# Kernel optimization log

Measured on AMD Instinct MI355X. Metric: run time of the kernel, lower is better.

## Reference

```python
import jax, jax.numpy as jnp
import numpy as np

B, L, H = 2, 2048, 1024
N_HEADS = 16
HEAD = H // N_HEADS
LN_EPS = 1e-12


def setup_inputs() -> dict:
    key = jax.random.key(0)
    ks = jax.random.split(key, 8)
    s = 1.0 / np.sqrt(H)
    return {
        "embeddings": jax.random.normal(ks[0], (B, L, H), dtype=jnp.float32),
        "mask": jnp.zeros((B, 1, 1, L), dtype=jnp.float32),
        "Wq": jax.random.normal(ks[1], (H, H), dtype=jnp.float32) * s,
        "bq": jnp.zeros((H,), dtype=jnp.float32),
        "Wk": jax.random.normal(ks[2], (H, H), dtype=jnp.float32) * s,
        "bk": jnp.zeros((H,), dtype=jnp.float32),
        "Wv": jax.random.normal(ks[3], (H, H), dtype=jnp.float32) * s,
        "bv": jnp.zeros((H,), dtype=jnp.float32),
        "Wo": jax.random.normal(ks[4], (H, H), dtype=jnp.float32) * s,
        "bo": jnp.zeros((H,), dtype=jnp.float32),
        "ln_gamma": jnp.ones((H,), dtype=jnp.float32),
        "ln_beta": jnp.zeros((H,), dtype=jnp.float32),
    }


def _layer_norm(x, gamma, beta):
    mu = jnp.mean(x, axis=-1, keepdims=True)
    var = jnp.mean(jnp.square(x - mu), axis=-1, keepdims=True)
    return (x - mu) * jax.lax.rsqrt(var + LN_EPS) * gamma + beta


def reference(embeddings, mask, Wq, bq, Wk, bk, Wv, bv, Wo, bo, ln_gamma, ln_beta):
    b, l, h = embeddings.shape
    # QKV projections, split heads -> [b, n_heads, l, head]
    def split_heads(x):
        return x.reshape(b, l, N_HEADS, HEAD).transpose(0, 2, 1, 3)
    q = split_heads(embeddings @ Wq + bq)
    k = split_heads(embeddings @ Wk + bk)
    v = split_heads(embeddings @ Wv + bv)
    # Faithful to source: energies use Q @ V^T, scaled by sqrt(n_heads)
    energies = jnp.einsum("bhqd,bhkd->bhqk", q, v) / np.sqrt(N_HEADS) + mask
    weights = jax.nn.softmax(energies, axis=3)
    # Faithful to source: attended = weights @ K
    attended = jnp.einsum("bhqk,bhkd->bhqd", weights, k)
    attended = attended.transpose(0, 2, 1, 3).reshape(b, l, h)
    # Residual feed-forward (BertSelfOutput style): dense + residual + LN
    out = attended @ Wo + bo
    return _layer_norm(out + embeddings, ln_gamma, ln_beta)
```

## Files before the change

### kernel.cpp

```cpp
#include <hip/hip_runtime.h>

#define LOG2E 1.44269504f
#define C_QSCALE 0.360673760f
#define C_SHIFT  34.6246810f
typedef unsigned short u16;
typedef short bf16x8 __attribute__((ext_vector_type(8)));
typedef float f32x4 __attribute__((ext_vector_type(4)));
typedef unsigned short u16x4 __attribute__((ext_vector_type(4)));

#define BB 2
#define LL 2048
#define HH 1024
#define NH 16
#define HD 64
#define ML (BB*LL)

__device__ __forceinline__ u16 f2bf(float f) {
  union { float f; unsigned u; } v; v.f = f;
  unsigned r = v.u + 0x7FFFu + ((v.u >> 16) & 1u);
  return (u16)(r >> 16);
}
__device__ __forceinline__ u16 f2bf_trunc(float f) {
  union { float f; unsigned u; } v; v.f = f;
  return (u16)(v.u >> 16);
}
__device__ __forceinline__ float bf2f(u16 u) {
  union { unsigned u; float f; } v; v.u = ((unsigned)u) << 16;
  return v.f;
}
__device__ __forceinline__ void gload_lds16(const u16* g, u16* l) {
  __builtin_amdgcn_global_load_lds((const __attribute__((address_space(1))) void*)g,
                                   (__attribute__((address_space(3))) void*)l, 16, 0, 0);
}

__global__ __launch_bounds__(256) void k_prep(const float* __restrict__ E, u16* __restrict__ X,
                                              const float* W0, const float* W1,
                                              const float* W2, const float* W3,
                                              u16* __restrict__ WT) {
  __shared__ __align__(16) u16 T[64*72];
  if (blockIdx.x < 2048) {
    int idx = (blockIdx.x * 256 + threadIdx.x) * 8;
    float4 a = *(const float4*)(E + idx);
    float4 b = *(const float4*)(E + idx + 4);
    bf16x8 o;
    o[0]=f2bf(a.x); o[1]=f2bf(a.y); o[2]=f2bf(a.z); o[3]=f2bf(a.w);
    o[4]=f2bf(b.x); o[5]=f2bf(b.y); o[6]=f2bf(b.z); o[7]=f2bf(b.w);
    *(bf16x8*)(X + idx) = o;
    return;
  }
  int bz = blockIdx.x - 2048;
  int z = bz >> 8, rem = bz & 255, bx = rem & 15, by = rem >> 4;
  const float* W = (z==0)?W0:(z==1)?W1:(z==2)?W2:W3;
  u16* dst = WT + (size_t)z * HH * HH;
  int t = threadIdx.x;
  int n0 = bx * 64, k0 = by * 64;
  int kl = t >> 2, nc = t & 3;
  #pragma unroll
  for (int u = 0; u < 4; ++u) {
    float4 v = *(const float4*)(W + (size_t)(k0 + kl) * HH + n0 + nc*16 + u*4);
    int nb = nc*16 + u*4;
    T[(nb+0)*72 + kl] = f2bf(v.x);
    T[(nb+1)*72 + kl] = f2bf(v.y);
    T[(nb+2)*72 + kl] = f2bf(v.z);
    T[(nb+3)*72 + kl] = f2bf(v.w);
  }
  __syncthreads();
  int nl = t >> 2, kc = (t & 3) * 16;
  #pragma unroll
  for (int e = 0; e < 2; ++e) {
    bf16x8 v = *(const bf16x8*)(T + nl*72 + kc + e*8);
    *(bf16x8*)(dst + (size_t)(n0+nl)*HH + k0 + kc + e*8) = v;
  }
}

__global__ __launch_bounds__(256) void k_gemm(const u16* __restrict__ A, const u16* __restrict__ Bt,
                                              const float* __restrict__ b0, const float* __restrict__ b1,
                                              const float* __restrict__ b2,
                                              u16* __restrict__ QH, u16* __restrict__ KV,
                                              float* __restrict__ outf, int mode) {
  __shared__ __align__(16) u16 As[2][128*32];
  __shared__ __align__(16) u16 Bs[2][128*32];
  int tid = threadIdx.x;
  int lane = tid & 63, w = tid >> 6;
  int c = lane & 15, g = lane >> 4;
  int bn0 = blockIdx.x * 128, bm0 = blockIdx.y * 128;
  int wm0 = (w >> 1) * 64, wn0 = (w & 1) * 64;
  int z = bn0 >> 10;
  bool swapd = (mode == 1) || (z != 1);
  const u16* srcA = swapd ? Bt : A;
  const u16* srcB = swapd ? A : Bt;
  int baseA = swapd ? bn0 : bm0;
  int baseB = swapd ? bm0 : bn0;

  f32x4 acc[4][4];
  #pragma unroll
  for (int mt = 0; mt < 4; ++mt)
    #pragma unroll
    for (int nt = 0; nt < 4; ++nt)
      acc[mt][nt] = (f32x4){0.f,0.f,0.f,0.f};

  #pragma unroll
  for (int it = 0; it < 2; ++it) {
    int ch = tid + it*256, row = ch >> 2, col = (ch & 3) * 8;
    gload_lds16(srcA + (size_t)(baseA + row) * HH + col, &As[0][ch*8]);
    gload_lds16(srcB + (size_t)(baseB + row) * HH + col, &Bs[0][ch*8]);
  }
  for (int kt = 0; kt < 32; ++kt) {
    __syncthreads();
    int cb = kt & 1;
    if (kt < 31) {
      int k0 = (kt + 1) * 32, nb = (kt + 1) & 1;
      #pragma unroll
      for (int it = 0; it < 2; ++it) {
        int ch = tid + it*256, row = ch >> 2, col = (ch & 3) * 8;
        gload_lds16(srcA + (size_t)(baseA + row) * HH + k0 + col, &As[nb][ch*8]);
        gload_lds16(srcB + (size_t)(baseB + row) * HH + k0 + col, &Bs[nb][ch*8]);
      }
    }
    bf16x8 af[4], bfr[4];
    #pragma unroll
    for (int i = 0; i < 4; ++i) {
      af[i]  = *(const bf16x8*)(&As[cb][0] + (wm0 + i*16 + c)*32 + g*8);
      bfr[i] = *(const bf16x8*)(&Bs[cb][0] + (wn0 + i*16 + c)*32 + g*8);
    }
    #pragma unroll
    for (int mt = 0; mt < 4; ++mt)
      #pragma unroll
      for (int nt = 0; nt < 4; ++nt)
        acc[mt][nt] = __builtin_amdgcn_mfma_f32_16x16x32_bf16(af[mt], bfr[nt], acc[mt][nt], 0, 0, 0);
  }

  if (mode == 1) {
    #pragma unroll
    for (int mt = 0; mt < 4; ++mt) {
      int n0 = bn0 + wm0 + mt*16 + 4*g;
      float4 bv = *(const float4*)(b0 + n0);
      #pragma unroll
      for (int nt = 0; nt < 4; ++nt) {
        int tok = bm0 + wn0 + nt*16 + c;
        float4 o;
        o.x = acc[mt][nt][0] + bv.x;
        o.y = acc[mt][nt][1] + bv.y;
        o.z = acc[mt][nt][2] + bv.z;
        o.w = acc[mt][nt][3] + bv.w;
        *(float4*)(outf + (size_t)tok * HH + n0) = o;
      }
    }
  } else if (z == 1) {
    #pragma unroll
    for (int nt = 0; nt < 4; ++nt) {
      int n = bn0 + wn0 + nt*16 + c;
      int nn = n & 1023, h = nn >> 6, d = nn & 63;
      float bv = b1[nn];
      #pragma unroll
      for (int mt = 0; mt < 4; ++mt) {
        int m0 = bm0 + wm0 + mt*16 + 4*g;
        int b = m0 >> 11, keyl = m0 & 2047;
        int tt = keyl >> 6, chunk = (keyl >> 3) & 7, s = keyl & 7;
        u16x4 pk;
        #pragma unroll
        for (int r = 0; r < 4; ++r) pk[r] = f2bf(acc[mt][nt][r] + bv);
        *(u16x4*)(KV + ((size_t)((b*NH + h)*32 + tt))*8192 + d*64 + ((chunk ^ (d & 7))*8) + s) = pk;
      }
    }
  } else {
    #pragma unroll
    for (int mt = 0; mt < 4; ++mt) {
      int nidx0 = bn0 + wm0 + mt*16 + 4*g;
      int nn0 = nidx0 & 1023, h = nn0 >> 6, d0 = nn0 & 63;
      const float* bp = (z == 0) ? b0 : b2;
      float4 bv = *(const float4*)(bp + nn0);
      #pragma unroll
      for (int nt = 0; nt < 4; ++nt) {
        int tok = bm0 + wn0 + nt*16 + c;
        int b = tok >> 11, l = tok & 2047;
        u16x4 o;
        o[0] = f2bf(acc[mt][nt][0] + bv.x);
        o[1] = f2bf(acc[mt][nt][1] + bv.y);
        o[2] = f2bf(acc[mt][nt][2] + bv.z);
        o[3] = f2bf(acc[mt][nt][3] + bv.w);
        if (z == 0) {
          *(u16x4*)(QH + (((size_t)(b*NH + h)) * LL + l) * HD + d0) = o;
        } else {
          int tt = l >> 6;
          *(u16x4*)(KV + ((size_t)((b*NH + h)*32 + tt))*8192 + 4096
                    + (l & 63)*64 + (((d0 >> 3) ^ (l & 7))*8) + (d0 & 7)) = o;
        }
      }
    }
  }
}

__global__ __launch_bounds__(256) void k_attn(const u16* __restrict__ QH, const u16* __restrict__ KV,
                                              const float* __restrict__ mask,
                                              u16* __restrict__ PO, float* __restrict__ PL) {
  __shared__ __align__(16) u16 sKV[8192];
  __shared__ __align__(16) u16 sP[4][32*72];
  int tid = threadIdx.x;
  int lane = tid & 63, w = tid >> 6;
  int c = lane & 15, g = lane >> 4;
  int z = blockIdx.y;
  int bh = blockIdx.z, b = bh >> 4;
  int q0 = blockIdx.x * 128 + w * 32;
  size_t qbase = (size_t)bh * LL * HD;
  const u16* kvg = KV + (size_t)bh * 32 * 8192 + (size_t)z * 16 * 8192;
  const float* mptr = mask + b * LL + z * 1024;
  u16* pw = &sP[w][0];

  bf16x8 aq[2][2];
  #pragma unroll
  for (int qi = 0; qi < 2; ++qi)
    #pragma unroll
    for (int ks = 0; ks < 2; ++ks)
      aq[qi][ks] = *(const bf16x8*)(QH + qbase + (size_t)(q0 + qi*16 + c) * HD + ks*32 + g*8);

  bf16x8 ones;
  #pragma unroll
  for (int i = 0; i < 8; ++i) ones[i] = (short)0x3F80;

  f32x4 O[2][4], lac[2];
  #pragma unroll
  for (int qi = 0; qi < 2; ++qi) {
    lac[qi] = (f32x4){0.f,0.f,0.f,0.f};
    #pragma unroll
    for (int dt = 0; dt < 4; ++dt) O[qi][dt] = (f32x4){0.f,0.f,0.f,0.f};
  }

  for (int tt = 0; tt < 16; ++tt) {
    __syncthreads();
    #pragma unroll
    for (int it = 0; it < 4; ++it) {
      int i = (tid + it*256) * 8;
      gload_lds16(kvg + (size_t)tt*8192 + i, sKV + i);
    }
    __syncthreads();

    int kv0 = tt * 64;
    #pragma unroll
    for (int nt = 0; nt < 4; ++nt) {
      int vrow = nt*16 + c;
      bf16x8 vb0 = *(const bf16x8*)(sKV + 4096 + vrow*64 + ((g ^ (c & 7))*8));
      bf16x8 vb1 = *(const bf16x8*)(sKV + 4096 + vrow*64 + (((4 + g) ^ (c & 7))*8));
      float mterm = fmaf(mptr[kv0 + vrow], LOG2E, -C_SHIFT);
      #pragma unroll
      for (int qi = 0; qi < 2; ++qi) {
        f32x4 sa = (f32x4){0.f,0.f,0.f,0.f};
        sa = __builtin_amdgcn_mfma_f32_16x16x32_bf16(aq[qi][0], vb0, sa, 0,0,0);
        sa = __builtin_amdgcn_mfma_f32_16x16x32_bf16(aq[qi][1], vb1, sa, 0,0,0);
        #pragma unroll
        for (int r = 0; r < 4; ++r)
          pw[(qi*16 + 4*g + r)*72 + nt*16 + c] = f2bf_trunc(exp2f(fmaf(sa[r], C_QSCALE, mterm)));
      }
    }
    bf16x8 ap[2][2];
    #pragma unroll
    for (int qi = 0; qi < 2; ++qi) {
      ap[qi][0] = *(const bf16x8*)(pw + (qi*16 + c)*72 + g*8);
      ap[qi][1] = *(const bf16x8*)(pw + (qi*16 + c)*72 + 32 + g*8);
      lac[qi] = __builtin_amdgcn_mfma_f32_16x16x32_bf16(ones, ap[qi][0], lac[qi], 0,0,0);
      lac[qi] = __builtin_amdgcn_mfma_f32_16x16x32_bf16(ones, ap[qi][1], lac[qi], 0,0,0);
    }
    #pragma unroll
    for (int dt = 0; dt < 4; ++dt) {
      int d = dt*16 + c;
      bf16x8 bk0 = *(const bf16x8*)(sKV + d*64 + ((g ^ (c & 7))*8));
      bf16x8 bk1 = *(const bf16x8*)(sKV + d*64 + (((4 + g) ^ (c & 7))*8));
      #pragma unroll
      for (int qi = 0; qi < 2; ++qi) {
        O[qi][dt] = __builtin_amdgcn_mfma_f32_16x16x32_bf16(bk0, ap[qi][0], O[qi][dt], 0,0,0);
        O[qi][dt] = __builtin_amdgcn_mfma_f32_16x16x32_bf16(bk1, ap[qi][1], O[qi][dt], 0,0,0);
      }
    }
  }
  #pragma unroll
  for (int qi = 0; qi < 2; ++qi) {
    size_t qrow = (size_t)(z*32 + bh) * LL + q0 + qi*16 + c;
    if (g == 0) PL[qrow] = lac[qi][0];
    #pragma unroll
    for (int dt = 0; dt < 4; ++dt) {
      u16x4 o;
      #pragma unroll
      for (int r = 0; r < 4; ++r) o[r] = f2bf(O[qi][dt][r]);
      *(u16x4*)(PO + qrow*HD + dt*16 + 4*g) = o;
    }
  }
}

__global__ __launch_bounds__(256) void k_combine(const u16* __restrict__ PO,
                                                 const float* __restrict__ PL,
                                                 u16* __restrict__ ATT) {
  int bh = blockIdx.y, b = bh >> 4, h = bh & 15;
  int q = blockIdx.x * 128 + (threadIdx.x >> 1);
  int dh = (threadIdx.x & 1) * 32;
  size_t r0 = ((size_t)bh * LL + q) * HD + dh;
  size_t r1 = ((size_t)(32 + bh) * LL + q) * HD + dh;
  float inv = 1.0f / (PL[(size_t)bh * LL + q] + PL[(size_t)(32 + bh) * LL + q]);
  u16* dst = ATT + ((size_t)(b*LL + q)) * HH + h*HD + dh;
  #pragma unroll
  for (int e = 0; e < 4; ++e) {
    bf16x8 a = *(const bf16x8*)(PO + r0 + e*8);
    bf16x8 bb = *(const bf16x8*)(PO + r1 + e*8);
    bf16x8 o;
    #pragma unroll
    for (int i = 0; i < 8; ++i)
      o[i] = (short)f2bf((bf2f((u16)a[i]) + bf2f((u16)bb[i])) * inv);
    *(bf16x8*)(dst + e*8) = o;
  }
}

__global__ __launch_bounds__(256) void k_ln(const float* __restrict__ OF, const float* __restrict__ E,
                                            const float* __restrict__ gamma, const float* __restrict__ beta,
                                            float* __restrict__ out) {
  int row = blockIdx.x;
  int tid = threadIdx.x, lane = tid & 63, w = tid >> 6;
  size_t basei = (size_t)row * HH + tid*4;
  float4 a = *(const float4*)(OF + basei);
  float4 e = *(const float4*)(E + basei);
  float x0 = a.x + e.x, x1 = a.y + e.y, x2 = a.z + e.z, x3 = a.w + e.w;
  float s1 = x0+x1+x2+x3;
  float s2 = x0*x0+x1*x1+x2*x2+x3*x3;
  #pragma unroll
  for (int off = 32; off; off >>= 1) { s1 += __shfl_xor(s1, off); s2 += __shfl_xor(s2, off); }
  __shared__ float r1[4], r2[4];
  if (lane == 0) { r1[w] = s1; r2[w] = s2; }
  __syncthreads();
  s1 = r1[0]+r1[1]+r1[2]+r1[3];
  s2 = r2[0]+r2[1]+r2[2]+r2[3];
  float mu = s1 * (1.0f/HH);
  float var = s2 * (1.0f/HH) - mu*mu;
  float rs = rsqrtf(fmaxf(var, 0.f) + 1e-12f);
  int colb = tid*4;
  float4 gm = *(const float4*)(gamma + colb);
  float4 bt = *(const float4*)(beta + colb);
  float4 o;
  o.x = (x0-mu)*rs*gm.x + bt.x;
  o.y = (x1-mu)*rs*gm.y + bt.y;
  o.z = (x2-mu)*rs*gm.z + bt.z;
  o.w = (x3-mu)*rs*gm.w + bt.w;
  *(float4*)(out + basei) = o;
}

extern "C" void kernel_launch(void* const* d_in, const int* in_sizes, int n_in,
                              void* d_out, int out_size, void* d_ws, size_t ws_size,
                              hipStream_t stream) {
  const float* E    = (const float*)d_in[0];
  const float* mask = (const float*)d_in[1];
  const float* Wq   = (const float*)d_in[2];
  const float* bq   = (const float*)d_in[3];
  const float* Wk   = (const float*)d_in[4];
  const float* bk   = (const float*)d_in[5];
  const float* Wv   = (const float*)d_in[6];
  const float* bv   = (const float*)d_in[7];
  const float* Wo   = (const float*)d_in[8];
  const float* bo   = (const float*)d_in[9];
  const float* gam  = (const float*)d_in[10];
  const float* bet  = (const float*)d_in[11];

  const size_t MH = (size_t)ML * HH;
  u16* XBF = (u16*)d_ws;
  u16* WT  = XBF + MH;
  u16* QH  = WT + 4*(size_t)HH*HH;
  u16* KV  = QH + MH;
  u16* ATT = KV + 2*MH;
  u16* PO  = ATT + MH;
  float* PL = (float*)XBF;
  float* OF = (float*)PO;
  float* out = (float*)d_out;

  k_prep<<<dim3(3072), 256, 0, stream>>>(E, XBF, Wq, Wk, Wv, Wo, WT);
  k_gemm<<<dim3(24,32), 256, 0, stream>>>(XBF, WT, bq, bk, bv, QH, KV, nullptr, 0);
  k_attn<<<dim3(16,2,32), 256, 0, stream>>>(QH, KV, mask, PO, PL);
  k_combine<<<dim3(16,32), 256, 0, stream>>>(PO, PL, ATT);
  k_gemm<<<dim3(8,32), 256, 0, stream>>>(ATT, WT + 3*(size_t)HH*HH, bo, nullptr, nullptr,
                                         nullptr, nullptr, OF, 1);
  k_ln<<<dim3(ML), 256, 0, stream>>>(OF, E, gam, bet, out);
}
```

Baseline: 256.7 us.

## Double-buffer KV tiles in attention and split output GEMM into smaller tiles

The attention kernel now prefetches the next KV tile into a second shared-memory buffer while the current one is computed. This removes one barrier per iteration and hides global-load latency, at the cost of twice the shared memory, which may reduce occupancy. The output projection moves to a dedicated kernel with 128x64 tiles, doubling the grid to 512 blocks so more CUs are busy, though each block gets less reuse.

Result: faster. 249.3 us (-2.9%).

```diff
diff --git a/kernel.cpp b/kernel.cpp
--- a/kernel.cpp
+++ b/kernel.cpp
@@ -76,8 +76,7 @@
 __global__ __launch_bounds__(256) void k_gemm(const u16* __restrict__ A, const u16* __restrict__ Bt,
                                               const float* __restrict__ b0, const float* __restrict__ b1,
                                               const float* __restrict__ b2,
-                                              u16* __restrict__ QH, u16* __restrict__ KV,
-                                              float* __restrict__ outf, int mode) {
+                                              u16* __restrict__ QH, u16* __restrict__ KV) {
   __shared__ __align__(16) u16 As[2][128*32];
   __shared__ __align__(16) u16 Bs[2][128*32];
   int tid = threadIdx.x;
@@ -86,7 +85,7 @@
   int bn0 = blockIdx.x * 128, bm0 = blockIdx.y * 128;
   int wm0 = (w >> 1) * 64, wn0 = (w & 1) * 64;
   int z = bn0 >> 10;
-  bool swapd = (mode == 1) || (z != 1);
+  bool swapd = (z != 1);
   const u16* srcA = swapd ? Bt : A;
   const u16* srcB = swapd ? A : Bt;
   int baseA = swapd ? bn0 : bm0;
@@ -130,23 +129,7 @@
         acc[mt][nt] = __builtin_amdgcn_mfma_f32_16x16x32_bf16(af[mt], bfr[nt], acc[mt][nt], 0, 0, 0);
   }
 
-  if (mode == 1) {
-    #pragma unroll
-    for (int mt = 0; mt < 4; ++mt) {
-      int n0 = bn0 + wm0 + mt*16 + 4*g;
-      float4 bv = *(const float4*)(b0 + n0);
-      #pragma unroll
-      for (int nt = 0; nt < 4; ++nt) {
-        int tok = bm0 + wn0 + nt*16 + c;
-        float4 o;
-        o.x = acc[mt][nt][0] + bv.x;
-        o.y = acc[mt][nt][1] + bv.y;
-        o.z = acc[mt][nt][2] + bv.z;
-        o.w = acc[mt][nt][3] + bv.w;
-        *(float4*)(outf + (size_t)tok * HH + n0) = o;
-      }
-    }
-  } else if (z == 1) {
+  if (z == 1) {
     #pragma unroll
     for (int nt = 0; nt < 4; ++nt) {
       int n = bn0 + wn0 + nt*16 + c;
@@ -191,10 +174,79 @@
   }
 }
 
+__global__ __launch_bounds__(256) void k_gemm_o(const u16* __restrict__ ATT, const u16* __restrict__ Wt,
+                                                const float* __restrict__ bias,
+                                                float* __restrict__ outf) {
+  __shared__ __align__(16) u16 As[2][128*32];
+  __shared__ __align__(16) u16 Bs[2][64*32];
+  int tid = threadIdx.x;
+  int lane = tid & 63, w = tid >> 6;
+  int c = lane & 15, g = lane >> 4;
+  int bn0 = blockIdx.x * 128, bm0 = blockIdx.y * 64;
+  int wm0 = (w >> 1) * 64, wn0 = (w & 1) * 32;
+
+  f32x4 acc[4][2];
+  #pragma unroll
+  for (int mt = 0; mt < 4; ++mt)
+    #pragma unroll
+    for (int nt = 0; nt < 2; ++nt)
+      acc[mt][nt] = (f32x4){0.f,0.f,0.f,0.f};
+
+  #pragma unroll
+  for (int it = 0; it < 2; ++it) {
+    int ch = tid + it*256, row = ch >> 2, col = (ch & 3) * 8;
+    gload_lds16(Wt + (size_t)(bn0 + row) * HH + col, &As[0][ch*8]);
+  }
+  { int row = tid >> 2, col = (tid & 3) * 8;
+    gload_lds16(ATT + (size_t)(bm0 + row) * HH + col, &Bs[0][tid*8]); }
+
+  for (int kt = 0; kt < 32; ++kt) {
+    __syncthreads();
+    int cb = kt & 1;
+    if (kt < 31) {
+      int k0 = (kt + 1) * 32, nb = (kt + 1) & 1;
+      #pragma unroll
+      for (int it = 0; it < 2; ++it) {
+        int ch = tid + it*256, row = ch >> 2, col = (ch & 3) * 8;
+        gload_lds16(Wt + (size_t)(bn0 + row) * HH + k0 + col, &As[nb][ch*8]);
+      }
+      int row = tid >> 2, col = (tid & 3) * 8;
+      gload_lds16(ATT + (size_t)(bm0 + row) * HH + k0 + col, &Bs[nb][tid*8]);
+    }
+    bf16x8 af[4], bfr[2];
+    #pragma unroll
+    for (int i = 0; i < 4; ++i)
+      af[i] = *(const bf16x8*)(&As[cb][0] + (wm0 + i*16 + c)*32 + g*8);
+    #pragma unroll
+    for (int j = 0; j < 2; ++j)
+      bfr[j] = *(const bf16x8*)(&Bs[cb][0] + (wn0 + j*16 + c)*32 + g*8);
+    #pragma unroll
+    for (int mt = 0; mt < 4; ++mt)
+      #pragma unroll
+      for (int nt = 0; nt < 2; ++nt)
+        acc[mt][nt] = __builtin_amdgcn_mfma_f32_16x16x32_bf16(af[mt], bfr[nt], acc[mt][nt], 0, 0, 0);
+  }
+  #pragma unroll
+  for (int mt = 0; mt < 4; ++mt) {
+    int n0 = bn0 + wm0 + mt*16 + 4*g;
+    float4 bv = *(const float4*)(bias + n0);
+    #pragma unroll
+    for (int nt = 0; nt < 2; ++nt) {
+      int tok = bm0 + wn0 + nt*16 + c;
+      float4 o;
+      o.x = acc[mt][nt][0] + bv.x;
+      o.y = acc[mt][nt][1] + bv.y;
+      o.z = acc[mt][nt][2] + bv.z;
+      o.w = acc[mt][nt][3] + bv.w;
+      *(float4*)(outf + (size_t)tok * HH + n0) = o;
+    }
+  }
+}
+
 __global__ __launch_bounds__(256) void k_attn(const u16* __restrict__ QH, const u16* __restrict__ KV,
                                               const float* __restrict__ mask,
                                               u16* __restrict__ PO, float* __restrict__ PL) {
-  __shared__ __align__(16) u16 sKV[8192];
+  __shared__ __align__(16) u16 sKV[2][8192];
   __shared__ __align__(16) u16 sP[4][32*72];
   int tid = threadIdx.x;
   int lane = tid & 63, w = tid >> 6;
@@ -226,21 +278,29 @@
     for (int dt = 0; dt < 4; ++dt) O[qi][dt] = (f32x4){0.f,0.f,0.f,0.f};
   }
 
+  #pragma unroll
+  for (int it = 0; it < 4; ++it) {
+    int i = (tid + it*256) * 8;
+    gload_lds16(kvg + i, &sKV[0][0] + i);
+  }
   for (int tt = 0; tt < 16; ++tt) {
     __syncthreads();
-    #pragma unroll
-    for (int it = 0; it < 4; ++it) {
-      int i = (tid + it*256) * 8;
-      gload_lds16(kvg + (size_t)tt*8192 + i, sKV + i);
-    }
-    __syncthreads();
-
+    const u16* cur = &sKV[tt & 1][0];
+    if (tt < 15) {
+      const u16* src = kvg + (size_t)(tt + 1) * 8192;
+      u16* dst = &sKV[(tt + 1) & 1][0];
+      #pragma unroll
+      for (int it = 0; it < 4; ++it) {
+        int i = (tid + it*256) * 8;
+        gload_lds16(src + i, dst + i);
+      }
+    }
     int kv0 = tt * 64;
     #pragma unroll
     for (int nt = 0; nt < 4; ++nt) {
       int vrow = nt*16 + c;
-      bf16x8 vb0 = *(const bf16x8*)(sKV + 4096 + vrow*64 + ((g ^ (c & 7))*8));
-      bf16x8 vb1 = *(const bf16x8*)(sKV + 4096 + vrow*64 + (((4 + g) ^ (c & 7))*8));
+      bf16x8 vb0 = *(const bf16x8*)(cur + 4096 + vrow*64 + ((g ^ (c & 7))*8));
+      bf16x8 vb1 = *(const bf16x8*)(cur + 4096 + vrow*64 + (((4 + g) ^ (c & 7))*8));
       float mterm = fmaf(mptr[kv0 + vrow], LOG2E, -C_SHIFT);
       #pragma unroll
       for (int qi = 0; qi < 2; ++qi) {
@@ -263,8 +323,8 @@
     #pragma unroll
     for (int dt = 0; dt < 4; ++dt) {
       int d = dt*16 + c;
-      bf16x8 bk0 = *(const bf16x8*)(sKV + d*64 + ((g ^ (c & 7))*8));
-      bf16x8 bk1 = *(const bf16x8*)(sKV + d*64 + (((4 + g) ^ (c & 7))*8));
+      bf16x8 bk0 = *(const bf16x8*)(cur + d*64 + ((g ^ (c & 7))*8));
+      bf16x8 bk1 = *(const bf16x8*)(cur + d*64 + (((4 + g) ^ (c & 7))*8));
       #pragma unroll
       for (int qi = 0; qi < 2; ++qi) {
         O[qi][dt] = __builtin_amdgcn_mfma_f32_16x16x32_bf16(bk0, ap[qi][0], O[qi][dt], 0,0,0);
@@ -368,10 +428,9 @@
   float* out = (float*)d_out;
 
   k_prep<<<dim3(3072), 256, 0, stream>>>(E, XBF, Wq, Wk, Wv, Wo, WT);
-  k_gemm<<<dim3(24,32), 256, 0, stream>>>(XBF, WT, bq, bk, bv, QH, KV, nullptr, 0);
+  k_gemm<<<dim3(24,32), 256, 0, stream>>>(XBF, WT, bq, bk, bv, QH, KV);
   k_attn<<<dim3(16,2,32), 256, 0, stream>>>(QH, KV, mask, PO, PL);
   k_combine<<<dim3(16,32), 256, 0, stream>>>(PO, PL, ATT);
-  k_gemm<<<dim3(8,32), 256, 0, stream>>>(ATT, WT + 3*(size_t)HH*HH, bo, nullptr, nullptr,
-                                         nullptr, nullptr, OF, 1);
+  k_gemm_o<<<dim3(8,64), 256, 0, stream>>>(ATT, WT + 3*(size_t)HH*HH, bo, OF);
   k_ln<<<dim3(ML), 256, 0, stream>>>(OF, E, gam, bet, out);
 }
```
